# Performance work log

Measured on AMD Instinct MI355X. Metric: run time of the kernel, lower is better.

## Reference

```python
import jax, jax.numpy as jnp
import numpy as np

N_GRID = 128
DX = 1.0 / N_GRID
INV_DX = float(N_GRID)
DT = 1e-4
P_VOL = (DX * 0.5) ** 2
P_RHO = 1.0
P_MASS = P_VOL * P_RHO
E_MOD, NU = 1000.0, 0.2
MU_0 = E_MOD / (2.0 * (1.0 + NU))
LAMBDA_0 = E_MOD * NU / ((1.0 + NU) * (1.0 - 2.0 * NU))
N_PART = 1_000_000


def setup_inputs() -> dict:
    key = jax.random.key(0)
    k1, k2, k3, k4, k5 = jax.random.split(key, 5)
    # particles strictly inside the domain so the 3x3 stencil stays in-grid
    x = 0.1 + 0.8 * jax.random.uniform(k1, (N_PART, 2), jnp.float32)
    v = 0.5 * jax.random.normal(k2, (N_PART, 2), jnp.float32)
    C = 0.1 * jax.random.normal(k3, (N_PART, 2, 2), jnp.float32)
    F = jnp.eye(2, dtype=jnp.float32)[None] + 0.01 * jax.random.normal(k4, (N_PART, 2, 2), jnp.float32)
    material = jax.random.randint(k5, (N_PART,), 0, 3, jnp.int32)
    Jp = jnp.ones((N_PART,), jnp.float32)
    return {"x": x, "v": v, "C": C, "F": F, "material": material, "Jp": Jp}


def mpm_step(x, v, C, F, material, Jp):
    # --- particle kinematics / constitutive model ---
    base = jnp.floor(x * INV_DX - 0.5).astype(jnp.int32)          # (N,2)
    fx = x * INV_DX - base.astype(x.dtype)                        # (N,2)
    w = jnp.stack([0.5 * (1.5 - fx) ** 2,
                   0.75 - (fx - 1.0) ** 2,
                   0.5 * (fx - 0.5) ** 2], axis=0)                # (3,N,2)

    F = F + DT * jnp.einsum('nij,njk->nik', C, F)
    m0 = material == 0
    m2 = material == 2
    h = jnp.where(material == 1, 0.3, jnp.exp(10.0 * (1.0 - Jp)))
    mu = jnp.where(m0, 0.0, MU_0 * h)
    lam = LAMBDA_0 * h

    U, sig, Vh = jnp.linalg.svd(F)                                # batched 2x2 SVD
    clamped = jnp.clip(sig, 1.0 - 2.5e-2, 1.0 + 4.5e-3)
    Jp = jnp.where(m2, Jp * jnp.prod(sig / clamped, axis=-1), Jp)
    sig = jnp.where(m2[:, None], clamped, sig)
    J = jnp.prod(sig, axis=-1)

    eye = jnp.eye(2, dtype=F.dtype)
    F_liquid = eye[None] * jnp.sqrt(J)[:, None, None]             # J**(1/n_dim), n_dim=2
    F_snow = jnp.einsum('nij,nj,njk->nik', U, sig, Vh)
    F = jnp.where(m0[:, None, None], F_liquid,
                  jnp.where(m2[:, None, None], F_snow, F))

    R = jnp.einsum('nij,njk->nik', U, Vh)
    stress = (2.0 * mu[:, None, None] * jnp.einsum('nij,nkj->nik', F - R, F)
              + eye[None] * (lam * J * (J - 1.0))[:, None, None])
    stress = (-DT * P_VOL * 4.0 * INV_DX ** 2) * stress
    affine = stress + P_MASS * C                                  # (N,2,2)

    mom = P_MASS * v - jnp.einsum('nij,nj->ni', affine, x)        # (N,2)

    # --- P2G scatter over 3x3 stencil ---
    grid_v = jnp.zeros((N_GRID * N_GRID, 2), x.dtype)
    grid_m = jnp.zeros((N_GRID * N_GRID,), x.dtype)
    grid_aff = jnp.zeros((N_GRID * N_GRID, 2, 2), x.dtype)
    for i in range(3):
        for j in range(3):
            weight = w[i, :, 0] * w[j, :, 1]                      # (N,)
            idx = (base[:, 0] + i) * N_GRID + (base[:, 1] + j)
            grid_v = grid_v.at[idx].add(weight[:, None] * mom)
            grid_aff = grid_aff.at[idx].add(weight[:, None, None] * affine)
            grid_m = grid_m.at[idx].add(weight * P_MASS)
    grid_v = grid_v.reshape(N_GRID, N_GRID, 2)
    grid_m = grid_m.reshape(N_GRID, N_GRID)
    grid_aff = grid_aff.reshape(N_GRID, N_GRID, 2, 2)

    gi = jnp.arange(N_GRID, dtype=x.dtype)
    grid_x = jnp.stack(jnp.meshgrid(gi, gi, indexing='ij'), axis=-1) * DX   # (G,G,2)
    grid_v = grid_v + jnp.einsum('abij,abj->abi', grid_aff, grid_x)

    # --- grid normalization, gravity, boundary clamps ---
    nonempty = grid_m > 0
    safe_m = jnp.where(nonempty, grid_m, 1.0)
    grid_v = jnp.where(nonempty[..., None], grid_v / safe_m[..., None], grid_v)
    grid_v = grid_v.at[:, :, 1].add(jnp.where(nonempty, -DT * 50.0, 0.0))

    row = jnp.arange(N_GRID)
    vx, vy = grid_v[..., 0], grid_v[..., 1]
    vx = jnp.where(row[:, None] < 3, jnp.maximum(vx, 0.0), vx)
    vx = jnp.where(row[:, None] >= N_GRID - 2, jnp.minimum(vx, 0.0), vx)
    vy = jnp.where(row[None, :] < 3, jnp.maximum(vy, 0.0), vy)
    vy = jnp.where(row[None, :] >= N_GRID - 2, jnp.minimum(vy, 0.0), vy)
    grid_v = jnp.stack([vx, vy], axis=-1)

    # --- G2P gather over 3x3 stencil ---
    new_v = jnp.zeros_like(v)
    new_C = jnp.zeros_like(C)
    for i in range(3):
        for j in range(3):
            weight = w[i, :, 0] * w[j, :, 1]
            g_v = grid_v[base[:, 0] + i, base[:, 1] + j]          # (N,2)
            node = (base + jnp.array([i, j], base.dtype)).astype(x.dtype) * DX
            new_v = new_v + weight[:, None] * g_v
            new_C = new_C + weight[:, None, None] * g_v[:, :, None] * node[:, None, :]
    new_C = (new_C - new_v[:, :, None] * x[:, None, :]) * (4.0 * INV_DX ** 2)

    x_new = x + DT * new_v
    return x_new, new_v, new_C, F, material, Jp


def reference(x, v, C, F, material, Jp):
    return mpm_step(x, v, C, F, material, Jp)
```

## Files before the change

### kernel.cpp

```cpp
#include <hip/hip_runtime.h>

#define NPART 1000000
#define NGRID 128
#define NNODES (NGRID * NGRID)
#define NBINS 64
#define BINCAP 26624
#define SUBW 18
#define SUBN (SUBW * SUBW)
#define P2G_SUB 8
#define P2G_THREADS 512
#define PS_CHUNK 4
#define PS_BLOCKS 977

#define FPSCALE 281474976710656.0f
#define FPINV   3.552713678800501e-15
#define WSCALE  16777216.0f
#define WINV    5.9604644775390625e-8

#define OUT_X   0
#define OUT_V   2000000
#define OUT_C   4000000
#define OUT_F   8000000
#define OUT_MAT 12000000
#define OUT_JP  13000000

__device__ __forceinline__ void quad_weights(float fx, float w[3]) {
    w[0] = 0.5f * (1.5f - fx) * (1.5f - fx);
    w[1] = 0.75f - (fx - 1.0f) * (fx - 1.0f);
    w[2] = 0.5f * (fx - 0.5f) * (fx - 0.5f);
}

struct PhysOut {
    float o00, o01, o10, o11;
    float aff00, aff01, aff10, aff11;
    float mom0, mom1;
    float jp_new;
};

__device__ __forceinline__ PhysOut particle_phys(
    float2 xx, float2 vv, float4 Cm, float4 Fin, int mat, float jp)
{
    const float DT = 1e-4f;
    const float P_MASS = 1.52587890625e-05f;
    const float MU_0 = (float)(1000.0 / (2.0 * 1.2));
    const float LAMBDA_0 = (float)(200.0 / 0.72);
    const float SCALE = -1e-4f;

    float F00 = Fin.x + DT * (Cm.x * Fin.x + Cm.y * Fin.z);
    float F01 = Fin.y + DT * (Cm.x * Fin.y + Cm.y * Fin.w);
    float F10 = Fin.z + DT * (Cm.z * Fin.x + Cm.w * Fin.z);
    float F11 = Fin.w + DT * (Cm.z * Fin.y + Cm.w * Fin.w);

    float h = (mat == 1) ? 0.3f : expf(10.0f * (1.0f - jp));
    float mu = (mat == 0) ? 0.0f : MU_0 * h;
    float lam = LAMBDA_0 * h;

    float Es = 0.5f * (F00 + F11), Fs = 0.5f * (F00 - F11);
    float Gs = 0.5f * (F01 + F10), Hs = 0.5f * (F10 - F01);
    float q2 = Es * Es + Hs * Hs;
    float r2 = Fs * Fs + Gs * Gs;
    float Qs = sqrtf(q2);
    float Rs = sqrtf(r2);
    float s1 = Qs + Rs, s2 = Qs - Rs;
    float cdif = 1.0f, sdif = 0.0f;
    if (q2 > 1e-30f) { float rq = 1.0f / Qs; cdif = Es * rq; sdif = Hs * rq; }
    float csum = 1.0f, ssum = 0.0f;
    if (r2 > 1e-30f) { float rr = 1.0f / Rs; csum = Fs * rr; ssum = Gs * rr; }
    float cucv = 0.5f * (cdif + csum);
    float susv = 0.5f * (cdif - csum);
    float cusv = 0.5f * (ssum - sdif);
    float sucv = 0.5f * (ssum + sdif);

    float c1 = fminf(fmaxf(s1, 1.0f - 2.5e-2f), 1.0f + 4.5e-3f);
    float c2 = fminf(fmaxf(s2, 1.0f - 2.5e-2f), 1.0f + 4.5e-3f);
    float jp_new = jp;
    float sg1 = s1, sg2 = s2;
    if (mat == 2) {
        jp_new = jp * (s1 / c1) * (s2 / c2);
        sg1 = c1;
        sg2 = c2;
    }
    float J = sg1 * sg2;

    float R00 = cdif, R01 = -sdif;
    float R10 = sdif, R11 = cdif;

    float o00, o01, o10, o11;
    if (mat == 0) {
        float sq = sqrtf(J);
        o00 = sq; o01 = 0.0f; o10 = 0.0f; o11 = sq;
    } else if (mat == 2) {
        o00 = sg1 * cucv + sg2 * susv;
        o01 = sg1 * cusv - sg2 * sucv;
        o10 = sg1 * sucv - sg2 * cusv;
        o11 = sg1 * susv + sg2 * cucv;
    } else {
        o00 = F00; o01 = F01; o10 = F10; o11 = F11;
    }

    float A00 = o00 - R00, A01 = o01 - R01, A10 = o10 - R10, A11 = o11 - R11;
    float S00 = A00 * o00 + A01 * o01;
    float S01 = A00 * o10 + A01 * o11;
    float S10 = A10 * o00 + A11 * o01;
    float S11 = A10 * o10 + A11 * o11;
    float ljj = lam * J * (J - 1.0f);

    PhysOut po;
    po.o00 = o00; po.o01 = o01; po.o10 = o10; po.o11 = o11;
    po.aff00 = SCALE * (2.0f * mu * S00 + ljj) + P_MASS * Cm.x;
    po.aff01 = SCALE * (2.0f * mu * S01)       + P_MASS * Cm.y;
    po.aff10 = SCALE * (2.0f * mu * S10)       + P_MASS * Cm.z;
    po.aff11 = SCALE * (2.0f * mu * S11 + ljj) + P_MASS * Cm.w;
    po.mom0 = P_MASS * vv.x - (po.aff00 * xx.x + po.aff01 * xx.y);
    po.mom1 = P_MASS * vv.y - (po.aff10 * xx.x + po.aff11 * xx.y);
    po.jp_new = jp_new;
    return po;
}

__device__ __forceinline__ int tile_of(float2 xx) {
    int b0 = (int)floorf(xx.x * 128.0f - 0.5f);
    int b1 = (int)floorf(xx.y * 128.0f - 0.5f);
    return ((b0 >> 4) << 3) | (b1 >> 4);
}

__global__ __launch_bounds__(256) void phys_scatter_kernel(
    const float2* __restrict__ x, const float2* __restrict__ v,
    const float4* __restrict__ C, const float4* __restrict__ F,
    const int* __restrict__ material, const float* __restrict__ Jp,
    int* __restrict__ binCursor, float* __restrict__ out, float4* __restrict__ rec)
{
    __shared__ int lh[NBINS];
    __shared__ int lbase[NBINS];
    int tid = threadIdx.x;
    if (tid < NBINS) lh[tid] = 0;
    __syncthreads();
    int base = blockIdx.x * (256 * PS_CHUNK);

    float2 xs[PS_CHUNK], vs[PS_CHUNK];
    float4 Cs[PS_CHUNK], Fs[PS_CHUNK];
    float jps[PS_CHUNK];
    int ms[PS_CHUNK], pk[PS_CHUNK];

    #pragma unroll
    for (int c = 0; c < PS_CHUNK; ++c) {
        int n = base + c * 256 + tid;
        if (n < NPART) {
            xs[c] = x[n]; vs[c] = v[n]; Cs[c] = C[n]; Fs[c] = F[n];
            ms[c] = material[n]; jps[c] = Jp[n];
            int t = tile_of(xs[c]);
            int r = atomicAdd(&lh[t], 1);
            pk[c] = (t << 16) | r;
        } else pk[c] = -1;
    }
    __syncthreads();
    if (tid < NBINS) {
        int c = lh[tid];
        lbase[tid] = c ? atomicAdd(&binCursor[tid], c) : 0;
    }
    __syncthreads();

    #pragma unroll
    for (int c = 0; c < PS_CHUNK; ++c) {
        if (pk[c] < 0) continue;
        int n = base + c * 256 + tid;
        PhysOut po = particle_phys(xs[c], vs[c], Cs[c], Fs[c], ms[c], jps[c]);
        ((float4*)(out + OUT_F))[n] = make_float4(po.o00, po.o01, po.o10, po.o11);
        out[OUT_MAT + n] = (float)ms[c];
        out[OUT_JP + n] = po.jp_new;
        int t = pk[c] >> 16, r = pk[c] & 0xffff;
        int pos = t * BINCAP + lbase[t] + r;
        rec[2 * pos]     = make_float4(xs[c].x, xs[c].y, po.mom0, po.mom1);
        rec[2 * pos + 1] = make_float4(po.aff00, po.aff01, po.aff10, po.aff11);
    }
}

__global__ __launch_bounds__(P2G_THREADS) void p2g_kernel(
    const float4* __restrict__ rec, const int* __restrict__ binCursor,
    float* __restrict__ part)
{
    __shared__ unsigned long long s_v0[SUBN], s_v1[SUBN];
    __shared__ unsigned int s_m[SUBN];
    int tid = threadIdx.x;
    int tile = blockIdx.x >> 3;
    int sub  = blockIdx.x & (P2G_SUB - 1);
    for (int i = tid; i < SUBN; i += P2G_THREADS) {
        s_v0[i] = 0ull; s_v1[i] = 0ull; s_m[i] = 0u;
    }
    __syncthreads();
    int start = tile * BINCAP;
    int cnt = binCursor[tile];
    int t0 = (tile >> 3) << 4;
    int t1 = (tile & 7) << 4;
    const float DX = 1.0f / 128.0f;

    for (int p = sub * P2G_THREADS + tid; p < cnt; p += P2G_SUB * P2G_THREADS) {
        float4 r0 = rec[2 * (start + p)];
        float4 r1 = rec[2 * (start + p) + 1];
        float xg0 = r0.x * 128.0f, xg1 = r0.y * 128.0f;
        int b0 = (int)floorf(xg0 - 0.5f), b1 = (int)floorf(xg1 - 0.5f);
        float fx0 = xg0 - (float)b0, fx1 = xg1 - (float)b1;
        float wx[3], wy[3];
        quad_weights(fx0, wx);
        quad_weights(fx1, wy);
        int l0 = b0 - t0, l1 = b1 - t1;
        #pragma unroll
        for (int i = 0; i < 3; ++i) {
            float nx0 = (float)(b0 + i) * DX;
            #pragma unroll
            for (int j = 0; j < 3; ++j) {
                float wt = wx[i] * wy[j];
                float nx1 = (float)(b1 + j) * DX;
                int l = (l0 + i) * SUBW + (l1 + j);
                long long q0 = (long long)(wt * (r0.z + r1.x * nx0 + r1.y * nx1) * FPSCALE);
                long long q1 = (long long)(wt * (r0.w + r1.z * nx0 + r1.w * nx1) * FPSCALE);
                unsigned int qm = (unsigned int)(wt * WSCALE);
                atomicAdd(&s_v0[l], (unsigned long long)q0);
                atomicAdd(&s_v1[l], (unsigned long long)q1);
                atomicAdd(&s_m[l], qm);
            }
        }
    }
    __syncthreads();
    float* slab = part + (size_t)blockIdx.x * (3 * SUBN);
    for (int l = tid; l < SUBN; l += P2G_THREADS) {
        slab[l]            = (float)((double)(long long)s_v0[l] * FPINV);
        slab[SUBN + l]     = (float)((double)(long long)s_v1[l] * FPINV);
        slab[2 * SUBN + l] = (float)((double)s_m[l] * WINV);
    }
}

__global__ __launch_bounds__(256) void grid_kernel(
    const float* __restrict__ part, float2* __restrict__ gvn)
{
    int idx = blockIdx.x * blockDim.x + threadIdx.x;
    if (idx >= NNODES) return;
    const float P_MASS = 1.52587890625e-05f;
    int gi = idx >> 7, gj = idx & 127;
    int li = gi & 15, lj = gj & 15, ti = gi >> 4, tj = gj >> 4;

    int tis[2], l0s[2]; int ni = 1; tis[0] = ti; l0s[0] = li;
    if (li < 2 && ti > 0) { tis[1] = ti - 1; l0s[1] = li + 16; ni = 2; }
    int tjs[2], l1s[2]; int nj = 1; tjs[0] = tj; l1s[0] = lj;
    if (lj < 2 && tj > 0) { tjs[1] = tj - 1; l1s[1] = lj + 16; nj = 2; }

    float s0 = 0.f, s1 = 0.f, sw = 0.f;
    for (int a = 0; a < ni; ++a) {
        for (int b = 0; b < nj; ++b) {
            int tile2 = tis[a] * 8 + tjs[b];
            int l = l0s[a] * SUBW + l1s[b];
            const float* sb = part + (size_t)(tile2 * P2G_SUB) * (3 * SUBN) + l;
            #pragma unroll
            for (int sub = 0; sub < P2G_SUB; ++sub) {
                s0 += sb[0];
                s1 += sb[SUBN];
                sw += sb[2 * SUBN];
                sb += 3 * SUBN;
            }
        }
    }
    float m = sw * P_MASS;
    if (m > 0.f) {
        float rm = 1.0f / m;
        s0 *= rm;
        s1 *= rm;
        s1 -= 5e-3f;
    }
    if (gi < 3) s0 = fmaxf(s0, 0.0f);
    if (gi >= NGRID - 2) s0 = fminf(s0, 0.0f);
    if (gj < 3) s1 = fmaxf(s1, 0.0f);
    if (gj >= NGRID - 2) s1 = fminf(s1, 0.0f);
    gvn[idx] = make_float2(s0, s1);
}

__global__ __launch_bounds__(256) void g2p_kernel(
    const float2* __restrict__ x, const float2* __restrict__ gvn,
    float* __restrict__ out)
{
    int n = blockIdx.x * blockDim.x + threadIdx.x;
    if (n >= NPART) return;
    const float DX = 1.0f / 128.0f;
    const float DT = 1e-4f;
    const float K4 = 65536.0f;

    float2 xx = x[n];
    float xg0 = xx.x * 128.0f, xg1 = xx.y * 128.0f;
    int b0 = (int)floorf(xg0 - 0.5f), b1 = (int)floorf(xg1 - 0.5f);
    float fx0 = xg0 - (float)b0, fx1 = xg1 - (float)b1;
    float wx[3], wy[3];
    quad_weights(fx0, wx);
    quad_weights(fx1, wy);

    float nv0 = 0.f, nv1 = 0.f;
    float nC00 = 0.f, nC01 = 0.f, nC10 = 0.f, nC11 = 0.f;
    #pragma unroll
    for (int i = 0; i < 3; ++i) {
        float node0 = (float)(b0 + i) * DX;
        #pragma unroll
        for (int j = 0; j < 3; ++j) {
            float wt = wx[i] * wy[j];
            float2 g = gvn[(b0 + i) * NGRID + (b1 + j)];
            float node1 = (float)(b1 + j) * DX;
            nv0 += wt * g.x;
            nv1 += wt * g.y;
            nC00 += wt * g.x * node0;
            nC01 += wt * g.x * node1;
            nC10 += wt * g.y * node0;
            nC11 += wt * g.y * node1;
        }
    }
    nC00 = (nC00 - nv0 * xx.x) * K4;
    nC01 = (nC01 - nv0 * xx.y) * K4;
    nC10 = (nC10 - nv1 * xx.x) * K4;
    nC11 = (nC11 - nv1 * xx.y) * K4;

    ((float2*)(out + OUT_X))[n] = make_float2(xx.x + DT * nv0, xx.y + DT * nv1);
    ((float2*)(out + OUT_V))[n] = make_float2(nv0, nv1);
    ((float4*)(out + OUT_C))[n] = make_float4(nC00, nC01, nC10, nC11);
}

extern "C" void kernel_launch(void* const* d_in, const int* in_sizes, int n_in,
                              void* d_out, int out_size, void* d_ws, size_t ws_size,
                              hipStream_t stream)
{
    const float2* x = (const float2*)d_in[0];
    const float2* v = (const float2*)d_in[1];
    const float4* C = (const float4*)d_in[2];
    const float4* F = (const float4*)d_in[3];
    const int* material = (const int*)d_in[4];
    const float* Jp = (const float*)d_in[5];
    float* out = (float*)d_out;

    int* binCursor = (int*)d_ws;
    float* part = (float*)((char*)d_ws + 4096);
    float2* gvn = (float2*)((char*)d_ws + (11 << 18));
    float4* rec = (float4*)((char*)d_ws + (4 << 20));

    hipMemsetAsync(binCursor, 0, NBINS * sizeof(int), stream);

    phys_scatter_kernel<<<PS_BLOCKS, 256, 0, stream>>>(x, v, C, F, material, Jp,
                                                       binCursor, out, rec);
    p2g_kernel<<<NBINS * P2G_SUB, P2G_THREADS, 0, stream>>>(rec, binCursor, part);
    grid_kernel<<<NNODES / 256, 256, 0, stream>>>(part, gvn);
    g2p_kernel<<<(NPART + 255) / 256, 256, 0, stream>>>(x, gvn, out);
}
```

Baseline: 173.4 us.

## Replicate P2G shared accumulators, split grid reduction across threads, halve scatter chunk

The P2G kernel now keeps two replicas of the shared-memory fixed-point accumulators, picked by wavefront parity, to cut atomic contention on hot grid nodes. The replicas are summed at writeout. The grid kernel gives each node eight threads, one per P2G sub-slab, and combines them with xor shuffles, which raises parallelism in that reduction. The phys/scatter kernel processes two particles per thread instead of four and launches twice as many blocks. The cost is double the shared memory in P2G, which may lower occupancy, plus extra shuffle work in the grid kernel.

```diff
diff --git a/kernel.cpp b/kernel.cpp
--- a/kernel.cpp
+++ b/kernel.cpp
@@ -9,8 +9,8 @@
 #define SUBN (SUBW * SUBW)
 #define P2G_SUB 8
 #define P2G_THREADS 512
-#define PS_CHUNK 4
-#define PS_BLOCKS 977
+#define PS_CHUNK 2
+#define PS_BLOCKS 1954
 
 #define FPSCALE 281474976710656.0f
 #define FPINV   3.552713678800501e-15
@@ -178,13 +178,15 @@
     const float4* __restrict__ rec, const int* __restrict__ binCursor,
     float* __restrict__ part)
 {
-    __shared__ unsigned long long s_v0[SUBN], s_v1[SUBN];
-    __shared__ unsigned int s_m[SUBN];
+    __shared__ unsigned long long s_v0[2][SUBN], s_v1[2][SUBN];
+    __shared__ unsigned int s_m[2][SUBN];
     int tid = threadIdx.x;
     int tile = blockIdx.x >> 3;
     int sub  = blockIdx.x & (P2G_SUB - 1);
-    for (int i = tid; i < SUBN; i += P2G_THREADS) {
-        s_v0[i] = 0ull; s_v1[i] = 0ull; s_m[i] = 0u;
+    int rep  = (tid >> 6) & 1;
+    for (int i = tid; i < 2 * SUBN; i += P2G_THREADS) {
+        int r = i >= SUBN, l = r ? i - SUBN : i;
+        s_v0[r][l] = 0ull; s_v1[r][l] = 0ull; s_m[r][l] = 0u;
     }
     __syncthreads();
     int start = tile * BINCAP;
@@ -214,25 +216,27 @@
                 long long q0 = (long long)(wt * (r0.z + r1.x * nx0 + r1.y * nx1) * FPSCALE);
                 long long q1 = (long long)(wt * (r0.w + r1.z * nx0 + r1.w * nx1) * FPSCALE);
                 unsigned int qm = (unsigned int)(wt * WSCALE);
-                atomicAdd(&s_v0[l], (unsigned long long)q0);
-                atomicAdd(&s_v1[l], (unsigned long long)q1);
-                atomicAdd(&s_m[l], qm);
+                atomicAdd(&s_v0[rep][l], (unsigned long long)q0);
+                atomicAdd(&s_v1[rep][l], (unsigned long long)q1);
+                atomicAdd(&s_m[rep][l], qm);
             }
         }
     }
     __syncthreads();
     float* slab = part + (size_t)blockIdx.x * (3 * SUBN);
     for (int l = tid; l < SUBN; l += P2G_THREADS) {
-        slab[l]            = (float)((double)(long long)s_v0[l] * FPINV);
-        slab[SUBN + l]     = (float)((double)(long long)s_v1[l] * FPINV);
-        slab[2 * SUBN + l] = (float)((double)s_m[l] * WINV);
+        slab[l]            = (float)((double)(long long)(s_v0[0][l] + s_v0[1][l]) * FPINV);
+        slab[SUBN + l]     = (float)((double)(long long)(s_v1[0][l] + s_v1[1][l]) * FPINV);
+        slab[2 * SUBN + l] = (float)((double)(s_m[0][l] + s_m[1][l]) * WINV);
     }
 }
 
 __global__ __launch_bounds__(256) void grid_kernel(
     const float* __restrict__ part, float2* __restrict__ gvn)
 {
-    int idx = blockIdx.x * blockDim.x + threadIdx.x;
+    int t = blockIdx.x * 256 + threadIdx.x;
+    int idx = t >> 3;
+    int sub = t & 7;
     if (idx >= NNODES) return;
     const float P_MASS = 1.52587890625e-05f;
     int gi = idx >> 7, gj = idx & 127;
@@ -248,28 +252,32 @@
         for (int b = 0; b < nj; ++b) {
             int tile2 = tis[a] * 8 + tjs[b];
             int l = l0s[a] * SUBW + l1s[b];
-            const float* sb = part + (size_t)(tile2 * P2G_SUB) * (3 * SUBN) + l;
-            #pragma unroll
-            for (int sub = 0; sub < P2G_SUB; ++sub) {
-                s0 += sb[0];
-                s1 += sb[SUBN];
-                sw += sb[2 * SUBN];
-                sb += 3 * SUBN;
-            }
+            const float* sb = part + (size_t)(tile2 * P2G_SUB + sub) * (3 * SUBN) + l;
+            s0 += sb[0];
+            s1 += sb[SUBN];
+            sw += sb[2 * SUBN];
         }
     }
-    float m = sw * P_MASS;
-    if (m > 0.f) {
-        float rm = 1.0f / m;
-        s0 *= rm;
-        s1 *= rm;
-        s1 -= 5e-3f;
-    }
-    if (gi < 3) s0 = fmaxf(s0, 0.0f);
-    if (gi >= NGRID - 2) s0 = fminf(s0, 0.0f);
-    if (gj < 3) s1 = fmaxf(s1, 0.0f);
-    if (gj >= NGRID - 2) s1 = fminf(s1, 0.0f);
-    gvn[idx] = make_float2(s0, s1);
+    #pragma unroll
+    for (int m = 4; m >= 1; m >>= 1) {
+        s0 += __shfl_xor(s0, m);
+        s1 += __shfl_xor(s1, m);
+        sw += __shfl_xor(sw, m);
+    }
+    if (sub == 0) {
+        float m = sw * P_MASS;
+        if (m > 0.f) {
+            float rm = 1.0f / m;
+            s0 *= rm;
+            s1 *= rm;
+            s1 -= 5e-3f;
+        }
+        if (gi < 3) s0 = fmaxf(s0, 0.0f);
+        if (gi >= NGRID - 2) s0 = fminf(s0, 0.0f);
+        if (gj < 3) s1 = fmaxf(s1, 0.0f);
+        if (gj >= NGRID - 2) s1 = fminf(s1, 0.0f);
+        gvn[idx] = make_float2(s0, s1);
+    }
 }
 
 __global__ __launch_bounds__(256) void g2p_kernel(
@@ -340,6 +348,6 @@
     phys_scatter_kernel<<<PS_BLOCKS, 256, 0, stream>>>(x, v, C, F, material, Jp,
                                                        binCursor, out, rec);
     p2g_kernel<<<NBINS * P2G_SUB, P2G_THREADS, 0, stream>>>(rec, binCursor, part);
-    grid_kernel<<<NNODES / 256, 256, 0, stream>>>(part, gvn);
+    grid_kernel<<<(NNODES * 8) / 256, 256, 0, stream>>>(part, gvn);
     g2p_kernel<<<(NPART + 255) / 256, 256, 0, stream>>>(x, gvn, out);
 }
```

New measurement: 186.2 us. 7.4% more time.
